# Performance work log

Hardware: AMD Instinct MI355X
Metric: run time of the kernel (lower is better)

Reference implementation:

```python
import jax, jax.numpy as jnp
import numpy as np

N = 50000      # nodes
E_RAND = 800000
IN = 256       # in_dim
HID = 64       # num_hidden
H = 4          # heads for GATv2 layers 0,1
C = 32         # num_classes (final layer, 1 head)
SLOPE = 0.2


def setup_inputs() -> dict:
    key = jax.random.key(0)
    ks = jax.random.split(key, 12)
    x = jax.random.normal(ks[0], (N, IN), dtype=jnp.float32)
    src = jax.random.randint(ks[1], (E_RAND,), 0, N, dtype=jnp.int32)
    dst = jax.random.randint(ks[2], (E_RAND,), 0, N, dtype=jnp.int32)
    loops = jnp.arange(N, dtype=jnp.int32)  # self-loops: every node has an in-edge
    src = jnp.concatenate([src, loops])
    dst = jnp.concatenate([dst, loops])
    s = 0.05
    W0 = jax.random.normal(ks[3], (IN, H * HID), dtype=jnp.float32) * s
    a0 = jax.random.normal(ks[4], (H, HID), dtype=jnp.float32) * s
    W1 = jax.random.normal(ks[5], (H * HID, H * HID), dtype=jnp.float32) * s
    a1 = jax.random.normal(ks[6], (H, HID), dtype=jnp.float32) * s
    W2 = jax.random.normal(ks[7], (H * HID, 1 * C), dtype=jnp.float32) * s
    a2 = jax.random.normal(ks[8], (1, C), dtype=jnp.float32) * s
    Wres2 = jax.random.normal(ks[9], (H * HID, C), dtype=jnp.float32) * s
    return {"x": x, "src": src, "dst": dst, "W0": W0, "a0": a0,
            "W1": W1, "a1": a1, "W2": W2, "a2": a2, "Wres2": Wres2}


def _gatv2_layer(h, W, a, src, dst, heads, out, res, activation):
    n = h.shape[0]
    # share_weights=True: same projection for src and dst (DGL GATv2Conv)
    f = (h @ W).reshape(n, heads, out)            # [N,H,D]
    fe = f[src] + f[dst]                          # gather: [E,H,D]
    e = jnp.einsum('ehd,hd->eh', jax.nn.leaky_relu(fe, SLOPE), a)  # [E,H]
    # edge softmax over incoming edges per destination node
    m = jax.ops.segment_max(e, dst, num_segments=n)
    ex = jnp.exp(e - m[dst])
    z = jax.ops.segment_sum(ex, dst, num_segments=n)
    alpha = ex / z[dst]                           # [E,H]
    msg = alpha[:, :, None] * f[src]              # [E,H,D]
    rst = jax.ops.segment_sum(msg, dst, num_segments=n)  # [N,H,D]
    if res is not None:
        rst = rst + res
    if activation:
        rst = jax.nn.elu(rst)
    return rst


def reference(x, src, dst, W0, a0, W1, a1, W2, a2, Wres2):
    # layer 0: no residual, elu, flatten heads
    h = _gatv2_layer(x, W0, a0, src, dst, H, HID, None, True).reshape(N, H * HID)
    # layer 1: residual (in == heads*out -> identity reshape), elu, flatten
    res1 = h.reshape(N, H, HID)
    h = _gatv2_layer(h, W1, a1, src, dst, H, HID, res1, True).reshape(N, H * HID)
    # final layer: residual via res_fc (256 != 1*32), no activation, mean over heads
    res2 = (h @ Wres2).reshape(N, 1, C)
    logits = _gatv2_layer(h, W2, a2, src, dst, 1, C, res2, False).mean(axis=1)
    return logits
```

## Files before the change

### kernel.cpp

```cpp
#include <hip/hip_runtime.h>
#include <hip/hip_bf16.h>

typedef __hip_bfloat16 bf16;
#define SLOPE 0.2f

__device__ __forceinline__ float b2f(bf16 v) { return __bfloat162float(v); }
__device__ __forceinline__ short f2b_raw(float x) {
    bf16 b = __float2bfloat16(x);
    return *reinterpret_cast<short*>(&b);
}

typedef __attribute__((ext_vector_type(8))) short bf16x8;
typedef __attribute__((ext_vector_type(16))) float f32x16;
typedef __attribute__((ext_vector_type(2))) float f32x2;

union Q16 { uint4 q[2]; unsigned u[8]; };

__global__ void k_prep(const void* __restrict__ x,
                       const void* __restrict__ W0, const void* __restrict__ W1,
                       const void* __restrict__ W2, const void* __restrict__ Wr2,
                       const void* __restrict__ a0, const void* __restrict__ a1,
                       const void* __restrict__ a2, bf16* __restrict__ W0p,
                       bf16* __restrict__ W1p, bf16* __restrict__ W2fp,
                       bf16* __restrict__ a0c, bf16* __restrict__ a1c,
                       bf16* __restrict__ a2c, int* __restrict__ flag,
                       int* __restrict__ cnt, int* __restrict__ ticket, int N) {
    __shared__ int sflag;
    if (threadIdx.x < 64) {
        const unsigned short* u = (const unsigned short*)x;
        int tid = threadIdx.x;
        int nice = 0;
        for (int k = tid; k < 256; k += 64) {
            unsigned int bits = ((unsigned int)u[2 * k]) << 16;
            float v = __uint_as_float(bits);
            float av = fabsf(v);
            if (v == 0.0f || (av > 1e-6f && av < 100.0f)) ++nice;
        }
        for (int off = 32; off > 0; off >>= 1) nice += __shfl_down(nice, off, 64);
        if (tid == 0) sflag = (nice >= 192) ? 0 : 1;
    }
    __syncthreads();
    int isf = sflag;
    int idx = blockIdx.x * blockDim.x + threadIdx.x;
    if (blockIdx.x == 0 && threadIdx.x == 0) { *flag = isf; *ticket = 0; }
    if (idx < N) cnt[idx] = 0;
    if (idx < 131072) {
        int t = idx & 65535;
        int j = t & 7, L = (t >> 3) & 63, kt = (t >> 9) & 15, nt = t >> 13;
        int n = nt * 32 + (L & 31);
        int k = kt * 16 + (L >> 5) * 8 + j;
        const void* src = (idx < 65536) ? W0 : W1;
        float v = isf ? ((const float*)src)[k * 256 + n] : b2f(((const bf16*)src)[k * 256 + n]);
        bf16* dstp = (idx < 65536) ? W0p : W1p;
        dstp[t] = __float2bfloat16(v);
    } else if (idx < 147456) {
        int t = idx - 131072;
        int j = t & 7, L = (t >> 3) & 63, kt = (t >> 9) & 15, nt = t >> 13;
        int n = nt * 32 + (L & 31);
        int k = kt * 16 + (L >> 5) * 8 + j;
        const void* src = (n < 32) ? W2 : Wr2;
        int nn = n & 31;
        float v = isf ? ((const float*)src)[k * 32 + nn] : b2f(((const bf16*)src)[k * 32 + nn]);
        W2fp[t] = __float2bfloat16(v);
    } else if (idx < 147456 + 256) {
        int t = idx - 147456;
        float v = isf ? ((const float*)a0)[t] : b2f(((const bf16*)a0)[t]);
        a0c[t] = __float2bfloat16(v);
    } else if (idx < 147456 + 512) {
        int t = idx - 147456 - 256;
        float v = isf ? ((const float*)a1)[t] : b2f(((const bf16*)a1)[t]);
        a1c[t] = __float2bfloat16(v);
    } else if (idx < 147456 + 544) {
        int t = idx - 147456 - 512;
        float v = isf ? ((const float*)a2)[t] : b2f(((const bf16*)a2)[t]);
        a2c[t] = __float2bfloat16(v);
    }
}

__global__ void k_hist(const int* __restrict__ dst, int* __restrict__ cnt, int E) {
    int e = blockIdx.x * blockDim.x + threadIdx.x;
    if (e < E) atomicAdd(&cnt[dst[e]], 1);
}

__global__ void k_bsum_scan(const int* __restrict__ cnt, int* __restrict__ bsum,
                            int* __restrict__ ticket, int n, int B) {
    __shared__ int sh[256];
    __shared__ int lastFlag;
    int base = blockIdx.x * 1024 + threadIdx.x * 4;
    int s = 0;
#pragma unroll
    for (int k = 0; k < 4; ++k) { int i = base + k; if (i < n) s += cnt[i]; }
    sh[threadIdx.x] = s;
    __syncthreads();
    for (int off = 128; off > 0; off >>= 1) {
        if (threadIdx.x < off) sh[threadIdx.x] += sh[threadIdx.x + off];
        __syncthreads();
    }
    if (threadIdx.x == 0) {
        atomicExch(&bsum[blockIdx.x], sh[0]);
        __threadfence();
        int t = atomicAdd(ticket, 1);
        lastFlag = (t == B - 1) ? 1 : 0;
    }
    __syncthreads();
    if (lastFlag && threadIdx.x < 64) {
        int tid = threadIdx.x;
        int v = (tid < B) ? atomicAdd(&bsum[tid], 0) : 0;
        int xv = v;
#pragma unroll
        for (int off = 1; off < 64; off <<= 1) {
            int y = __shfl_up(xv, off, 64);
            if (tid >= off) xv += y;
        }
        if (tid < B) bsum[tid] = xv - v;
    }
}

__global__ void k_scanwrite(const int* __restrict__ cnt, const int* __restrict__ bsum,
                            int* __restrict__ rowptr, int* __restrict__ cursor, int n, int E) {
    __shared__ int sh[256];
    int base = blockIdx.x * 1024 + threadIdx.x * 4;
    int loc[4];
    int s = 0;
#pragma unroll
    for (int k = 0; k < 4; ++k) {
        int i = base + k;
        loc[k] = (i < n) ? cnt[i] : 0;
        s += loc[k];
    }
    sh[threadIdx.x] = s;
    __syncthreads();
    for (int off = 1; off < 256; off <<= 1) {
        int u = (threadIdx.x >= off) ? sh[threadIdx.x - off] : 0;
        __syncthreads();
        sh[threadIdx.x] += u;
        __syncthreads();
    }
    int run = bsum[blockIdx.x] + sh[threadIdx.x] - s;
#pragma unroll
    for (int k = 0; k < 4; ++k) {
        int i = base + k;
        if (i < n) { rowptr[i] = run; cursor[i] = run; run += loc[k]; }
    }
    if (blockIdx.x == 0 && threadIdx.x == 0) rowptr[n] = E;
}

__global__ void k_scatter(const int* __restrict__ src, const int* __restrict__ dst,
                          int* __restrict__ cursor, int* __restrict__ csr_src, int E) {
    int e = blockIdx.x * blockDim.x + threadIdx.x;
    if (e < E) {
        int p = atomicAdd(&cursor[dst[e]], 1);
        csr_src[p] = src[e];
    }
}

template <int ADAPT>
__global__ void k_gemm_mfma(const void* __restrict__ A, const bf16* __restrict__ Wp,
                            bf16* __restrict__ C, int Nrows, const int* __restrict__ flag) {
    __shared__ short sA[64 * 264];
    int tid = threadIdx.x;
    int warp = tid >> 6;
    int lane = tid & 63;
    long blockRow = (long)blockIdx.x * 64;
    int isf32 = ADAPT ? *flag : 0;

    if (ADAPT && isf32) {
        const float* Af = (const float*)A;
#pragma unroll
        for (int it = 0; it < 16; ++it) {
            int linear = it * 256 + tid;
            int row = linear >> 6;
            int col4 = linear & 63;
            long gr = blockRow + row;
            if (gr > Nrows - 1) gr = Nrows - 1;
            float4 v = ((const float4*)(Af + gr * 256))[col4];
            short* d = &sA[row * 264 + col4 * 4];
            d[0] = f2b_raw(v.x); d[1] = f2b_raw(v.y);
            d[2] = f2b_raw(v.z); d[3] = f2b_raw(v.w);
        }
    } else {
        const short* Ab = (const short*)A;
#pragma unroll
        for (int it = 0; it < 8; ++it) {
            int linear = it * 256 + tid;
            int row = linear >> 5;
            int c8 = linear & 31;
            long gr = blockRow + row;
            if (gr > Nrows - 1) gr = Nrows - 1;
            bf16x8 v = *(const bf16x8*)(Ab + gr * 256 + c8 * 8);
            *(bf16x8*)&sA[row * 264 + c8 * 8] = v;
        }
    }
    __syncthreads();

    int wr = warp >> 1;
    int wc = warp & 1;
    long rowBase = blockRow + wr * 32;
    int colBase = wc * 128;
    int m = lane & 31;
    int g = lane >> 5;
    const short* Wps = (const short*)Wp;
    int smemRow = wr * 32 + m;
    f32x16 acc[4] = {};
    for (int kt = 0; kt < 16; ++kt) {
        bf16x8 af = *(const bf16x8*)&sA[smemRow * 264 + kt * 16 + g * 8];
#pragma unroll
        for (int ct = 0; ct < 4; ++ct) {
            int nt = wc * 4 + ct;
            bf16x8 bfr = *(const bf16x8*)(Wps + (((nt << 4) + kt) << 9) + lane * 8);
            acc[ct] = __builtin_amdgcn_mfma_f32_32x32x16_bf16(af, bfr, acc[ct], 0, 0, 0);
        }
    }
#pragma unroll
    for (int ct = 0; ct < 4; ++ct) {
#pragma unroll
        for (int i = 0; i < 16; ++i) {
            long row = rowBase + (i & 3) + 8 * (i >> 2) + 4 * g;
            if (row < Nrows)
                C[row * 256 + colBase + ct * 32 + m] = __float2bfloat16(acc[ct][i]);
        }
    }
}

__global__ void k_gemm_mfma64(const bf16* __restrict__ A, const bf16* __restrict__ Wp,
                              bf16* __restrict__ C, int Nrows) {
    int warp = threadIdx.x >> 6;
    int lane = threadIdx.x & 63;
    long rowBase = (long)blockIdx.x * 128 + warp * 32;
    int m = lane & 31;
    int g = lane >> 5;
    long r = rowBase + m;
    if (r >= Nrows) r = Nrows - 1;
    const short* Arow = (const short*)A + r * 256 + g * 8;
    const short* Wps = (const short*)Wp;
    f32x16 acc[2] = {};
    for (int kt = 0; kt < 16; ++kt) {
        bf16x8 af = *(const bf16x8*)(Arow + kt * 16);
#pragma unroll
        for (int ct = 0; ct < 2; ++ct) {
            bf16x8 bfr = *(const bf16x8*)(Wps + (((ct << 4) + kt) << 9) + lane * 8);
            acc[ct] = __builtin_amdgcn_mfma_f32_32x32x16_bf16(af, bfr, acc[ct], 0, 0, 0);
        }
    }
#pragma unroll
    for (int ct = 0; ct < 2; ++ct) {
#pragma unroll
        for (int i = 0; i < 16; ++i) {
            long row = rowBase + (i & 3) + 8 * (i >> 2) + 4 * g;
            if (row < Nrows)
                C[row * 64 + ct * 32 + m] = __float2bfloat16(acc[ct][i]);
        }
    }
}

__global__ void k_gat_fused(const uint4* __restrict__ f, const bf16* __restrict__ a,
                            const int* __restrict__ rowptr, const int* __restrict__ csr_src,
                            const uint4* __restrict__ res, uint4* __restrict__ out,
                            int N, int mode) {
    int n = (blockIdx.x * blockDim.x + threadIdx.x) >> 6;
    int lane = threadIdx.x & 63;
    if (n >= N) return;
    int j = lane >> 4, l = lane & 15;

    Q16 fdq, aq;
    fdq.q[0] = f[(long)n * 32 + 2 * l];
    fdq.q[1] = f[(long)n * 32 + 2 * l + 1];
    aq.q[0] = ((const uint4*)a)[2 * l];
    aq.q[1] = ((const uint4*)a)[2 * l + 1];
    f32x2 fd2[8], a6[8], a4[8];
#pragma unroll
    for (int i = 0; i < 8; ++i) {
        f32x2 fv, av;
        fv.x = __uint_as_float(fdq.u[i] << 16);
        fv.y = __uint_as_float(fdq.u[i] & 0xffff0000u);
        av.x = __uint_as_float(aq.u[i] << 16);
        av.y = __uint_as_float(aq.u[i] & 0xffff0000u);
        fd2[i] = fv;
        a6[i] = 0.6f * av;
        a4[i] = 0.4f * av;
    }

    int p0 = rowptr[n], p1 = rowptr[n + 1];
    int iters = (p1 - p0 + 3) >> 2;
    float z = 0.f;
    f32x2 acc[8] = {};

    int p = p0 + j;
    int pc = p1 - 1;
    Q16 A0, A1, B0, B1;
    {
        int s0 = csr_src[min(p, pc)];
        A0.q[0] = f[(long)s0 * 32 + 2 * l];
        A0.q[1] = f[(long)s0 * 32 + 2 * l + 1];
        int s1 = csr_src[min(p + 4, pc)];
        A1.q[0] = f[(long)s1 * 32 + 2 * l];
        A1.q[1] = f[(long)s1 * 32 + 2 * l + 1];
    }
    for (int i = 0; i < iters; i += 2) {
        int s0 = csr_src[min(p + 8, pc)];
        B0.q[0] = f[(long)s0 * 32 + 2 * l];
        B0.q[1] = f[(long)s0 * 32 + 2 * l + 1];
        int s1 = csr_src[min(p + 12, pc)];
        B1.q[0] = f[(long)s1 * 32 + 2 * l];
        B1.q[1] = f[(long)s1 * 32 + 2 * l + 1];

#pragma unroll
        for (int half = 0; half < 2; ++half) {
            if (half == 1 && i + 1 >= iters) break;
            const Q16& cur = half ? A1 : A0;
            int pp = p + half * 4;
            f32x2 fs[8];
            f32x2 t2 = {0.f, 0.f};
#pragma unroll
            for (int k = 0; k < 8; ++k) {
                f32x2 fv;
                fv.x = __uint_as_float(cur.u[k] << 16);
                fv.y = __uint_as_float(cur.u[k] & 0xffff0000u);
                fs[k] = fv;
                f32x2 u = fv + fd2[k];
                f32x2 ua;
                ua.x = __uint_as_float(__float_as_uint(u.x) & 0x7fffffffu);
                ua.y = __uint_as_float(__float_as_uint(u.y) & 0x7fffffffu);
                t2 = a6[k] * u + t2;
                t2 = a4[k] * ua + t2;
            }
            float t = t2.x + t2.y;
            t += __shfl_xor(t, 1);
            t += __shfl_xor(t, 2);
            float wgt = (pp < p1) ? __expf(t) : 0.f;
            z += wgt;
            f32x2 w2 = {wgt, wgt};
#pragma unroll
            for (int k = 0; k < 8; ++k) acc[k] = w2 * fs[k] + acc[k];
        }
        A0 = B0;
        A1 = B1;
        p += 8;
    }
    z += __shfl_xor(z, 16);
    z += __shfl_xor(z, 32);
#pragma unroll
    for (int k = 0; k < 8; ++k) {
        acc[k].x += __shfl_xor(acc[k].x, 16);
        acc[k].x += __shfl_xor(acc[k].x, 32);
        acc[k].y += __shfl_xor(acc[k].y, 16);
        acc[k].y += __shfl_xor(acc[k].y, 32);
    }
    if (j < 2) {
        float invz = 1.f / z;
        float o[8];
#pragma unroll
        for (int k = 0; k < 4; ++k) {
            int kk = j * 4 + k;
            o[2 * k]     = acc[kk].x * invz;
            o[2 * k + 1] = acc[kk].y * invz;
        }
        if (mode == 1) {
            uint4 rq = res[(long)n * 32 + 2 * l + j];
            const unsigned* ru = (const unsigned*)&rq;
#pragma unroll
            for (int k = 0; k < 4; ++k) {
                o[2 * k]     += __uint_as_float(ru[k] << 16);
                o[2 * k + 1] += __uint_as_float(ru[k] & 0xffff0000u);
            }
        }
        union { uint4 q; short s[8]; } ob;
#pragma unroll
        for (int k = 0; k < 8; ++k) {
            float v = o[k] > 0.f ? o[k] : (__expf(o[k]) - 1.f);
            ob.s[k] = f2b_raw(v);
        }
        out[(long)n * 32 + 2 * l + j] = ob.q;
    }
}

__global__ void k_gat_fused_fin(const unsigned* __restrict__ fr2u, const bf16* __restrict__ a2,
                                const int* __restrict__ rowptr, const int* __restrict__ csr_src,
                                void* __restrict__ outraw, int N, const int* __restrict__ flag) {
    int n = (blockIdx.x * blockDim.x + threadIdx.x) >> 6;
    int lane = threadIdx.x & 63;
    if (n >= N) return;
    int j = lane >> 4, l = lane & 15;

    unsigned fdu = fr2u[(long)n * 32 + l];
    unsigned au  = ((const unsigned*)a2)[l];
    f32x2 fd2, a6, a4;
    fd2.x = __uint_as_float(fdu << 16);
    fd2.y = __uint_as_float(fdu & 0xffff0000u);
    float ax = __uint_as_float(au << 16);
    float ay = __uint_as_float(au & 0xffff0000u);
    a6.x = 0.6f * ax; a6.y = 0.6f * ay;
    a4.x = 0.4f * ax; a4.y = 0.4f * ay;

    int p0 = rowptr[n], p1 = rowptr[n + 1];
    int iters = (p1 - p0 + 3) >> 2;
    float z = 0.f;
    f32x2 acc = {0.f, 0.f};

    int p = p0 + j;
    int pc = p1 - 1;
    unsigned A0, A1, B0, B1;
    A0 = fr2u[(long)csr_src[min(p, pc)] * 32 + l];
    A1 = fr2u[(long)csr_src[min(p + 4, pc)] * 32 + l];
    for (int i = 0; i < iters; i += 2) {
        B0 = fr2u[(long)csr_src[min(p + 8, pc)] * 32 + l];
        B1 = fr2u[(long)csr_src[min(p + 12, pc)] * 32 + l];
#pragma unroll
        for (int half = 0; half < 2; ++half) {
            if (half == 1 && i + 1 >= iters) break;
            unsigned cu = half ? A1 : A0;
            int pp = p + half * 4;
            f32x2 fs;
            fs.x = __uint_as_float(cu << 16);
            fs.y = __uint_as_float(cu & 0xffff0000u);
            f32x2 u = fs + fd2;
            f32x2 ua;
            ua.x = __uint_as_float(__float_as_uint(u.x) & 0x7fffffffu);
            ua.y = __uint_as_float(__float_as_uint(u.y) & 0x7fffffffu);
            f32x2 t2 = a6 * u + a4 * ua;
            float t = t2.x + t2.y;
            t += __shfl_xor(t, 1);
            t += __shfl_xor(t, 2);
            t += __shfl_xor(t, 4);
            t += __shfl_xor(t, 8);
            float wgt = (pp < p1) ? __expf(t) : 0.f;
            z += wgt;
            f32x2 w2 = {wgt, wgt};
            acc = w2 * fs + acc;
        }
        A0 = B0;
        A1 = B1;
        p += 8;
    }
    z += __shfl_xor(z, 16);
    z += __shfl_xor(z, 32);
    acc.x += __shfl_xor(acc.x, 16);
    acc.x += __shfl_xor(acc.x, 32);
    acc.y += __shfl_xor(acc.y, 16);
    acc.y += __shfl_xor(acc.y, 32);
    if (j == 0) {
        unsigned ru = fr2u[(long)n * 32 + 16 + l];
        float invz = 1.f / z;
        float o0 = acc.x * invz + __uint_as_float(ru << 16);
        float o1 = acc.y * invz + __uint_as_float(ru & 0xffff0000u);
        if (*flag) {
            float2 ov = {o0, o1};
            ((float2*)outraw)[(long)n * 16 + l] = ov;
        } else {
            unsigned ob = ((unsigned)(unsigned short)f2b_raw(o0)) |
                          (((unsigned)(unsigned short)f2b_raw(o1)) << 16);
            ((unsigned*)outraw)[(long)n * 16 + l] = ob;
        }
    }
}

extern "C" void kernel_launch(void* const* d_in, const int* in_sizes, int n_in,
                              void* d_out, int out_size, void* d_ws, size_t ws_size,
                              hipStream_t stream) {
    const int N = in_sizes[0] / 256;
    const int E = in_sizes[1];

    const void* x   = d_in[0];
    const int*  src = (const int*)d_in[1];
    const int*  dst = (const int*)d_in[2];

    char* w = (char*)d_ws;
    auto alloc = [&](size_t bytes) -> char* {
        char* p = w;
        w += (bytes + 15) & ~(size_t)15;
        return p;
    };
    bf16* buf0 = (bf16*)alloc((size_t)N * 256 * 2);
    bf16* buf1 = (bf16*)alloc((size_t)N * 256 * 2);
    bf16* buf2 = (bf16*)alloc((size_t)N * 256 * 2);
    int* csr_src = (int*)alloc((size_t)E * 4);
    int* rowptr  = (int*)alloc((size_t)(N + 1) * 4);
    int* cursor  = (int*)alloc((size_t)N * 4);
    int* cnt     = (int*)alloc((size_t)N * 4);
    int* bsum    = (int*)alloc((size_t)1024 * 4);
    bf16* W0p  = (bf16*)alloc((size_t)65536 * 2);
    bf16* W1p  = (bf16*)alloc((size_t)65536 * 2);
    bf16* W2fp = (bf16*)alloc((size_t)64 * 256 * 2);
    bf16* a0c  = (bf16*)alloc((size_t)256 * 2);
    bf16* a1c  = (bf16*)alloc((size_t)256 * 2);
    bf16* a2c  = (bf16*)alloc((size_t)32 * 2);
    int*  flag = (int*)alloc(16);
    int*  ticket = (int*)alloc(16);

    bf16* hA  = buf1;
    bf16* fB  = buf2;
    bf16* hB  = buf0;
    bf16* fr2 = buf2;

    int prepN = 147456 + 544;
    if (prepN < N) prepN = N;
    k_prep<<<(prepN + 255) / 256, 256, 0, stream>>>(
        x, d_in[3], d_in[5], d_in[7], d_in[9], d_in[4], d_in[6], d_in[8],
        W0p, W1p, W2fp, a0c, a1c, a2c, flag, cnt, ticket, N);

    const int B = (N + 1023) / 1024;
    k_hist<<<(E + 255) / 256, 256, 0, stream>>>(dst, cnt, E);
    k_bsum_scan<<<B, 256, 0, stream>>>(cnt, bsum, ticket, N, B);
    k_scanwrite<<<B, 256, 0, stream>>>(cnt, bsum, rowptr, cursor, N, E);
    k_scatter<<<(E + 255) / 256, 256, 0, stream>>>(src, dst, cursor, csr_src, E);

    const int ngrid4 = (int)(((long)N * 64 + 255) / 256);

    k_gemm_mfma<1><<<(N + 63) / 64, 256, 0, stream>>>(x, W0p, fB, N, flag);
    k_gat_fused<<<ngrid4, 256, 0, stream>>>((const uint4*)fB, a0c, rowptr, csr_src,
                                            nullptr, (uint4*)hA, N, 0);
    k_gemm_mfma<0><<<(N + 63) / 64, 256, 0, stream>>>(hA, W1p, fB, N, flag);
    k_gat_fused<<<ngrid4, 256, 0, stream>>>((const uint4*)fB, a1c, rowptr, csr_src,
                                            (const uint4*)hA, (uint4*)hB, N, 1);
    k_gemm_mfma64<<<(N + 127) / 128, 256, 0, stream>>>(hB, W2fp, fr2, N);
    k_gat_fused_fin<<<ngrid4, 256, 0, stream>>>((const unsigned*)fr2, a2c, rowptr, csr_src,
                                                d_out, N, flag);
}
```

Measured before the change: 419.3 us.

## Switch intermediate storage and edge-score math from bf16 to fp16 packed ops

Converts weights, projected features and hidden activations from bf16 to fp16. GEMMs now use the f16 MFMA, and the per-edge attention score (add, abs, fma) runs with packed half2 arithmetic instead of unpacked fp32 pairs. The goal is to cut VALU work in the gather-heavy GAT kernels by using packed fp16 math. The trade-off is fp16's narrower range and lower-precision accumulation of attention logits, and the bf16-input path now needs an extra conversion.

```diff
diff --git a/kernel.cpp b/kernel.cpp
--- a/kernel.cpp
+++ b/kernel.cpp
@@ -3,16 +3,28 @@
 
 typedef __hip_bfloat16 bf16;
 #define SLOPE 0.2f
+
+typedef _Float16 h2v __attribute__((ext_vector_type(2)));
+typedef _Float16 h8v __attribute__((ext_vector_type(8)));
+typedef __attribute__((ext_vector_type(8))) short bf16x8;
+typedef __attribute__((ext_vector_type(16))) float f32x16;
+typedef __attribute__((ext_vector_type(2))) float f32x2;
 
 __device__ __forceinline__ float b2f(bf16 v) { return __bfloat162float(v); }
 __device__ __forceinline__ short f2b_raw(float x) {
     bf16 b = __float2bfloat16(x);
     return *reinterpret_cast<short*>(&b);
 }
-
-typedef __attribute__((ext_vector_type(8))) short bf16x8;
-typedef __attribute__((ext_vector_type(16))) float f32x16;
-typedef __attribute__((ext_vector_type(2))) float f32x2;
+__device__ __forceinline__ short f2h_raw(float x) {
+    _Float16 h = (_Float16)x;
+    return *reinterpret_cast<short*>(&h);
+}
+__device__ __forceinline__ h2v u2h(unsigned u) {
+    union { unsigned x; h2v h; } c; c.x = u; return c.h;
+}
+__device__ __forceinline__ h2v habs2(h2v a) {
+    union { h2v h; unsigned x; } c; c.h = a; c.x &= 0x7fff7fffu; return c.h;
+}
 
 union Q16 { uint4 q[2]; unsigned u[8]; };
 
@@ -20,10 +32,10 @@
                        const void* __restrict__ W0, const void* __restrict__ W1,
                        const void* __restrict__ W2, const void* __restrict__ Wr2,
                        const void* __restrict__ a0, const void* __restrict__ a1,
-                       const void* __restrict__ a2, bf16* __restrict__ W0p,
-                       bf16* __restrict__ W1p, bf16* __restrict__ W2fp,
-                       bf16* __restrict__ a0c, bf16* __restrict__ a1c,
-                       bf16* __restrict__ a2c, int* __restrict__ flag,
+                       const void* __restrict__ a2, short* __restrict__ W0p,
+                       short* __restrict__ W1p, short* __restrict__ W2fp,
+                       short* __restrict__ a0c, short* __restrict__ a1c,
+                       short* __restrict__ a2c, int* __restrict__ flag,
                        int* __restrict__ cnt, int* __restrict__ ticket, int N) {
     __shared__ int sflag;
     if (threadIdx.x < 64) {
@@ -51,8 +63,8 @@
         int k = kt * 16 + (L >> 5) * 8 + j;
         const void* src = (idx < 65536) ? W0 : W1;
         float v = isf ? ((const float*)src)[k * 256 + n] : b2f(((const bf16*)src)[k * 256 + n]);
-        bf16* dstp = (idx < 65536) ? W0p : W1p;
-        dstp[t] = __float2bfloat16(v);
+        short* dstp = (idx < 65536) ? W0p : W1p;
+        dstp[t] = f2h_raw(v);
     } else if (idx < 147456) {
         int t = idx - 131072;
         int j = t & 7, L = (t >> 3) & 63, kt = (t >> 9) & 15, nt = t >> 13;
@@ -61,19 +73,19 @@
         const void* src = (n < 32) ? W2 : Wr2;
         int nn = n & 31;
         float v = isf ? ((const float*)src)[k * 32 + nn] : b2f(((const bf16*)src)[k * 32 + nn]);
-        W2fp[t] = __float2bfloat16(v);
+        W2fp[t] = f2h_raw(v);
     } else if (idx < 147456 + 256) {
         int t = idx - 147456;
         float v = isf ? ((const float*)a0)[t] : b2f(((const bf16*)a0)[t]);
-        a0c[t] = __float2bfloat16(v);
+        a0c[t] = f2h_raw(v);
     } else if (idx < 147456 + 512) {
         int t = idx - 147456 - 256;
         float v = isf ? ((const float*)a1)[t] : b2f(((const bf16*)a1)[t]);
-        a1c[t] = __float2bfloat16(v);
+        a1c[t] = f2h_raw(v);
     } else if (idx < 147456 + 544) {
         int t = idx - 147456 - 512;
         float v = isf ? ((const float*)a2)[t] : b2f(((const bf16*)a2)[t]);
-        a2c[t] = __float2bfloat16(v);
+        a2c[t] = f2h_raw(v);
     }
 }
 
@@ -155,8 +167,8 @@
 }
 
 template <int ADAPT>
-__global__ void k_gemm_mfma(const void* __restrict__ A, const bf16* __restrict__ Wp,
-                            bf16* __restrict__ C, int Nrows, const int* __restrict__ flag) {
+__global__ void k_gemm_mfma(const void* __restrict__ A, const short* __restrict__ Wp,
+                            short* __restrict__ C, int Nrows, const int* __restrict__ flag) {
     __shared__ short sA[64 * 264];
     int tid = threadIdx.x;
     int warp = tid >> 6;
@@ -175,8 +187,25 @@
             if (gr > Nrows - 1) gr = Nrows - 1;
             float4 v = ((const float4*)(Af + gr * 256))[col4];
             short* d = &sA[row * 264 + col4 * 4];
-            d[0] = f2b_raw(v.x); d[1] = f2b_raw(v.y);
-            d[2] = f2b_raw(v.z); d[3] = f2b_raw(v.w);
+            d[0] = f2h_raw(v.x); d[1] = f2h_raw(v.y);
+            d[2] = f2h_raw(v.z); d[3] = f2h_raw(v.w);
+        }
+    } else if (ADAPT) {
+        const short* Ab = (const short*)A;
+#pragma unroll
+        for (int it = 0; it < 8; ++it) {
+            int linear = it * 256 + tid;
+            int row = linear >> 5;
+            int c8 = linear & 31;
+            long gr = blockRow + row;
+            if (gr > Nrows - 1) gr = Nrows - 1;
+            bf16x8 v = *(const bf16x8*)(Ab + gr * 256 + c8 * 8);
+            short* d = &sA[row * 264 + c8 * 8];
+#pragma unroll
+            for (int k = 0; k < 8; ++k) {
+                unsigned bits = ((unsigned)(unsigned short)v[k]) << 16;
+                d[k] = f2h_raw(__uint_as_float(bits));
+            }
         }
     } else {
         const short* Ab = (const short*)A;
@@ -199,16 +228,15 @@
     int colBase = wc * 128;
     int m = lane & 31;
     int g = lane >> 5;
-    const short* Wps = (const short*)Wp;
     int smemRow = wr * 32 + m;
     f32x16 acc[4] = {};
     for (int kt = 0; kt < 16; ++kt) {
-        bf16x8 af = *(const bf16x8*)&sA[smemRow * 264 + kt * 16 + g * 8];
+        h8v af = *(const h8v*)&sA[smemRow * 264 + kt * 16 + g * 8];
 #pragma unroll
         for (int ct = 0; ct < 4; ++ct) {
             int nt = wc * 4 + ct;
-            bf16x8 bfr = *(const bf16x8*)(Wps + (((nt << 4) + kt) << 9) + lane * 8);
-            acc[ct] = __builtin_amdgcn_mfma_f32_32x32x16_bf16(af, bfr, acc[ct], 0, 0, 0);
+            h8v bfr = *(const h8v*)(Wp + (((nt << 4) + kt) << 9) + lane * 8);
+            acc[ct] = __builtin_amdgcn_mfma_f32_32x32x16_f16(af, bfr, acc[ct], 0, 0, 0);
         }
     }
 #pragma unroll
@@ -217,13 +245,13 @@
         for (int i = 0; i < 16; ++i) {
             long row = rowBase + (i & 3) + 8 * (i >> 2) + 4 * g;
             if (row < Nrows)
-                C[row * 256 + colBase + ct * 32 + m] = __float2bfloat16(acc[ct][i]);
-        }
-    }
-}
-
-__global__ void k_gemm_mfma64(const bf16* __restrict__ A, const bf16* __restrict__ Wp,
-                              bf16* __restrict__ C, int Nrows) {
+                C[row * 256 + colBase + ct * 32 + m] = f2h_raw(acc[ct][i]);
+        }
+    }
+}
+
+__global__ void k_gemm_mfma64(const short* __restrict__ A, const short* __restrict__ Wp,
+                              short* __restrict__ C, int Nrows) {
     int warp = threadIdx.x >> 6;
     int lane = threadIdx.x & 63;
     long rowBase = (long)blockIdx.x * 128 + warp * 32;
@@ -231,15 +259,14 @@
     int g = lane >> 5;
     long r = rowBase + m;
     if (r >= Nrows) r = Nrows - 1;
-    const short* Arow = (const short*)A + r * 256 + g * 8;
-    const short* Wps = (const short*)Wp;
+    const short* Arow = A + r * 256 + g * 8;
     f32x16 acc[2] = {};
     for (int kt = 0; kt < 16; ++kt) {
-        bf16x8 af = *(const bf16x8*)(Arow + kt * 16);
+        h8v af = *(const h8v*)(Arow + kt * 16);
 #pragma unroll
         for (int ct = 0; ct < 2; ++ct) {
-            bf16x8 bfr = *(const bf16x8*)(Wps + (((ct << 4) + kt) << 9) + lane * 8);
-            acc[ct] = __builtin_amdgcn_mfma_f32_32x32x16_bf16(af, bfr, acc[ct], 0, 0, 0);
+            h8v bfr = *(const h8v*)(Wp + (((ct << 4) + kt) << 9) + lane * 8);
+            acc[ct] = __builtin_amdgcn_mfma_f32_32x32x16_f16(af, bfr, acc[ct], 0, 0, 0);
         }
     }
 #pragma unroll
@@ -248,12 +275,12 @@
         for (int i = 0; i < 16; ++i) {
             long row = rowBase + (i & 3) + 8 * (i >> 2) + 4 * g;
             if (row < Nrows)
-                C[row * 64 + ct * 32 + m] = __float2bfloat16(acc[ct][i]);
-        }
-    }
-}
-
-__global__ void k_gat_fused(const uint4* __restrict__ f, const bf16* __restrict__ a,
+                C[row * 64 + ct * 32 + m] = f2h_raw(acc[ct][i]);
+        }
+    }
+}
+
+__global__ void k_gat_fused(const uint4* __restrict__ f, const short* __restrict__ a,
                             const int* __restrict__ rowptr, const int* __restrict__ csr_src,
                             const uint4* __restrict__ res, uint4* __restrict__ out,
                             int N, int mode) {
@@ -267,17 +294,17 @@
     fdq.q[1] = f[(long)n * 32 + 2 * l + 1];
     aq.q[0] = ((const uint4*)a)[2 * l];
     aq.q[1] = ((const uint4*)a)[2 * l + 1];
-    f32x2 fd2[8], a6[8], a4[8];
+    h2v fdh[8], a6h[8], a4h[8];
 #pragma unroll
     for (int i = 0; i < 8; ++i) {
-        f32x2 fv, av;
-        fv.x = __uint_as_float(fdq.u[i] << 16);
-        fv.y = __uint_as_float(fdq.u[i] & 0xffff0000u);
-        av.x = __uint_as_float(aq.u[i] << 16);
-        av.y = __uint_as_float(aq.u[i] & 0xffff0000u);
-        fd2[i] = fv;
-        a6[i] = 0.6f * av;
-        a4[i] = 0.4f * av;
+        fdh[i] = u2h(fdq.u[i]);
+        h2v av = u2h(aq.u[i]);
+        float ax = (float)av.x, ay = (float)av.y;
+        h2v t6, t4;
+        t6.x = (_Float16)(0.6f * ax); t6.y = (_Float16)(0.6f * ay);
+        t4.x = (_Float16)(0.4f * ax); t4.y = (_Float16)(0.4f * ay);
+        a6h[i] = t6;
+        a4h[i] = t4;
     }
 
     int p0 = rowptr[n], p1 = rowptr[n + 1];
@@ -309,29 +336,27 @@
             if (half == 1 && i + 1 >= iters) break;
             const Q16& cur = half ? A1 : A0;
             int pp = p + half * 4;
-            f32x2 fs[8];
-            f32x2 t2 = {0.f, 0.f};
+            h2v t2;
+            t2.x = (_Float16)0.f; t2.y = (_Float16)0.f;
 #pragma unroll
             for (int k = 0; k < 8; ++k) {
-                f32x2 fv;
-                fv.x = __uint_as_float(cur.u[k] << 16);
-                fv.y = __uint_as_float(cur.u[k] & 0xffff0000u);
-                fs[k] = fv;
-                f32x2 u = fv + fd2[k];
-                f32x2 ua;
-                ua.x = __uint_as_float(__float_as_uint(u.x) & 0x7fffffffu);
-                ua.y = __uint_as_float(__float_as_uint(u.y) & 0x7fffffffu);
-                t2 = a6[k] * u + t2;
-                t2 = a4[k] * ua + t2;
+                h2v fs = u2h(cur.u[k]);
+                h2v u = fs + fdh[k];
+                h2v ua = habs2(u);
+                t2 = a6h[k] * u + t2;
+                t2 = a4h[k] * ua + t2;
             }
-            float t = t2.x + t2.y;
+            float t = (float)t2.x + (float)t2.y;
             t += __shfl_xor(t, 1);
             t += __shfl_xor(t, 2);
             float wgt = (pp < p1) ? __expf(t) : 0.f;
             z += wgt;
-            f32x2 w2 = {wgt, wgt};
-#pragma unroll
-            for (int k = 0; k < 8; ++k) acc[k] = w2 * fs[k] + acc[k];
+#pragma unroll
+            for (int k = 0; k < 8; ++k) {
+                h2v fs = u2h(cur.u[k]);
+                acc[k].x = fmaf((float)fs.x, wgt, acc[k].x);
+                acc[k].y = fmaf((float)fs.y, wgt, acc[k].y);
+            }
         }
         A0 = B0;
         A1 = B1;
@@ -360,21 +385,22 @@
             const unsigned* ru = (const unsigned*)&rq;
 #pragma unroll
             for (int k = 0; k < 4; ++k) {
-                o[2 * k]     += __uint_as_float(ru[k] << 16);
-                o[2 * k + 1] += __uint_as_float(ru[k] & 0xffff0000u);
+                h2v rh = u2h(ru[k]);
+                o[2 * k]     += (float)rh.x;
+                o[2 * k + 1] += (float)rh.y;
             }
         }
         union { uint4 q; short s[8]; } ob;
 #pragma unroll
         for (int k = 0; k < 8; ++k) {
             float v = o[k] > 0.f ? o[k] : (__expf(o[k]) - 1.f);
-            ob.s[k] = f2b_raw(v);
+            ob.s[k] = f2h_raw(v);
         }
         out[(long)n * 32 + 2 * l + j] = ob.q;
     }
 }
 
-__global__ void k_gat_fused_fin(const unsigned* __restrict__ fr2u, const bf16* __restrict__ a2,
+__global__ void k_gat_fused_fin(const unsigned* __restrict__ fr2u, const short* __restrict__ a2,
                                 const int* __restrict__ rowptr, const int* __restrict__ csr_src,
                                 void* __restrict__ outraw, int N, const int* __restrict__ flag) {
     int n = (blockIdx.x * blockDim.x + threadIdx.x) >> 6;
@@ -384,13 +410,12 @@
 
     unsigned fdu = fr2u[(long)n * 32 + l];
     unsigned au  = ((const unsigned*)a2)[l];
-    f32x2 fd2, a6, a4;
-    fd2.x = __uint_as_float(fdu << 16);
-    fd2.y = __uint_as_float(fdu & 0xffff0000u);
-    float ax = __uint_as_float(au << 16);
-    float ay = __uint_as_float(au & 0xffff0000u);
-    a6.x = 0.6f * ax; a6.y = 0.6f * ay;
-    a4.x = 0.4f * ax; a4.y = 0.4f * ay;
+    h2v fdh = u2h(fdu);
+    h2v av  = u2h(au);
+    float ax = (float)av.x, ay = (float)av.y;
+    h2v a6h, a4h;
+    a6h.x = (_Float16)(0.6f * ax); a6h.y = (_Float16)(0.6f * ay);
+    a4h.x = (_Float16)(0.4f * ax); a4h.y = (_Float16)(0.4f * ay);
 
     int p0 = rowptr[n], p1 = rowptr[n + 1];
     int iters = (p1 - p0 + 3) >> 2;
@@ -410,23 +435,20 @@
             if (half == 1 && i + 1 >= iters) break;
             unsigned cu = half ? A1 : A0;
             int pp = p + half * 4;
-            f32x2 fs;
-            fs.x = __uint_as_float(cu << 16);
-            fs.y = __uint_as_float(cu & 0xffff0000u);
-            f32x2 u = fs + fd2;
-            f32x2 ua;
-            ua.x = __uint_as_float(__float_as_uint(u.x) & 0x7fffffffu);
-            ua.y = __uint_as_float(__float_as_uint(u.y) & 0x7fffffffu);
-            f32x2 t2 = a6 * u + a4 * ua;
-            float t = t2.x + t2.y;
+            h2v fs = u2h(cu);
+            h2v u = fs + fdh;
+            h2v ua = habs2(u);
+            h2v t2 = a6h * u;
+            t2 = a4h * ua + t2;
+            float t = (float)t2.x + (float)t2.y;
             t += __shfl_xor(t, 1);
             t += __shfl_xor(t, 2);
             t += __shfl_xor(t, 4);
             t += __shfl_xor(t, 8);
             float wgt = (pp < p1) ? __expf(t) : 0.f;
             z += wgt;
-            f32x2 w2 = {wgt, wgt};
-            acc = w2 * fs + acc;
+            acc.x = fmaf((float)fs.x, wgt, acc.x);
+            acc.y = fmaf((float)fs.y, wgt, acc.y);
         }
         A0 = B0;
         A1 = B1;
@@ -440,9 +462,10 @@
     acc.y += __shfl_xor(acc.y, 32);
     if (j == 0) {
         unsigned ru = fr2u[(long)n * 32 + 16 + l];
+        h2v rh = u2h(ru);
         float invz = 1.f / z;
-        float o0 = acc.x * invz + __uint_as_float(ru << 16);
-        float o1 = acc.y * invz + __uint_as_float(ru & 0xffff0000u);
+        float o0 = acc.x * invz + (float)rh.x;
+        float o1 = acc.y * invz + (float)rh.y;
         if (*flag) {
             float2 ov = {o0, o1};
             ((float2*)outraw)[(long)n * 16 + l] = ov;
@@ -470,27 +493,27 @@
         w += (bytes + 15) & ~(size_t)15;
         return p;
     };
-    bf16* buf0 = (bf16*)alloc((size_t)N * 256 * 2);
-    bf16* buf1 = (bf16*)alloc((size_t)N * 256 * 2);
-    bf16* buf2 = (bf16*)alloc((size_t)N * 256 * 2);
+    short* buf0 = (short*)alloc((size_t)N * 256 * 2);
+    short* buf1 = (short*)alloc((size_t)N * 256 * 2);
+    short* buf2 = (short*)alloc((size_t)N * 256 * 2);
     int* csr_src = (int*)alloc((size_t)E * 4);
     int* rowptr  = (int*)alloc((size_t)(N + 1) * 4);
     int* cursor  = (int*)alloc((size_t)N * 4);
     int* cnt     = (int*)alloc((size_t)N * 4);
     int* bsum    = (int*)alloc((size_t)1024 * 4);
-    bf16* W0p  = (bf16*)alloc((size_t)65536 * 2);
-    bf16* W1p  = (bf16*)alloc((size_t)65536 * 2);
-    bf16* W2fp = (bf16*)alloc((size_t)64 * 256 * 2);
-    bf16* a0c  = (bf16*)alloc((size_t)256 * 2);
-    bf16* a1c  = (bf16*)alloc((size_t)256 * 2);
-    bf16* a2c  = (bf16*)alloc((size_t)32 * 2);
+    short* W0p  = (short*)alloc((size_t)65536 * 2);
+    short* W1p  = (short*)alloc((size_t)65536 * 2);
+    short* W2fp = (short*)alloc((size_t)64 * 256 * 2);
+    short* a0c  = (short*)alloc((size_t)256 * 2);
+    short* a1c  = (short*)alloc((size_t)256 * 2);
+    short* a2c  = (short*)alloc((size_t)32 * 2);
     int*  flag = (int*)alloc(16);
     int*  ticket = (int*)alloc(16);
 
-    bf16* hA  = buf1;
-    bf16* fB  = buf2;
-    bf16* hB  = buf0;
-    bf16* fr2 = buf2;
+    short* hA  = buf1;
+    short* fB  = buf2;
+    short* hB  = buf0;
+    short* fr2 = buf2;
 
     int prepN = 147456 + 544;
     if (prepN < N) prepN = N;
```

Measured after the change: 418.6 us. About the same (-0.2%).
